# Kernel optimization log

Measured on AMD Instinct MI355X. Metric: run time of the kernel, lower is better.

The kernel has to match this reference:

```python
import jax, jax.numpy as jnp
import numpy as np

N, E, F, H, C1 = 50000, 1_600_000, 48, 1, 16  # nodes, edges, in_feats, heads, conv out


def setup_inputs() -> dict:
    key = jax.random.key(0)
    ks = jax.random.split(key, 12)
    in_ = jax.random.normal(ks[0], (N, F), dtype=jnp.float32)
    edge_index = jax.random.randint(ks[1], (2, E), 0, N, dtype=jnp.int64)
    labels = jax.random.bernoulli(ks[2], 0.5, (N, 1)).astype(jnp.float32)
    weights = jax.random.uniform(ks[3], (N, 1), dtype=jnp.float32) + 0.5
    s = 0.1  # PyG FeaStConv init: normal(0, 0.1)
    W = jax.random.normal(ks[4], (F, H * C1), dtype=jnp.float32) * s
    u = jax.random.normal(ks[5], (F, H), dtype=jnp.float32) * s
    c = jax.random.normal(ks[6], (H,), dtype=jnp.float32) * s
    bias = jax.random.normal(ks[7], (C1,), dtype=jnp.float32) * s
    lin1_w = jax.random.normal(ks[8], (C1, 8), dtype=jnp.float32) * (1.0 / np.sqrt(C1))
    lin1_b = jnp.zeros((8,), dtype=jnp.float32)
    out_w = jax.random.normal(ks[9], (8, 1), dtype=jnp.float32) * (1.0 / np.sqrt(8))
    out_b = jnp.zeros((1,), dtype=jnp.float32)
    return {"in_": in_, "edge_index": edge_index, "labels": labels,
            "weights": weights, "W": W, "u": u, "c": c, "bias": bias,
            "lin1_w": lin1_w, "lin1_b": lin1_b, "out_w": out_w, "out_b": out_b}


def feast_conv(x, edge_index, W, u, c, bias):
    n = x.shape[0]
    loop = jnp.arange(n, dtype=edge_index.dtype)  # add_self_loops=True
    src = jnp.concatenate([edge_index[0], loop])
    dst = jnp.concatenate([edge_index[1], loop])
    xj = x[src]                                   # [E+N, F] gather
    xi = x[dst]
    q = jax.nn.softmax((xj - xi) @ u + c, axis=-1)            # [E+N, H]
    xw = (xj @ W).reshape(-1, H, C1)                           # [E+N, H, C1]
    msg = jnp.einsum('ehc,eh->ec', xw, q)                      # [E+N, C1]
    agg = jax.ops.segment_sum(msg, dst, num_segments=n)        # scatter-sum
    deg = jax.ops.segment_sum(jnp.ones_like(dst, dtype=x.dtype), dst, num_segments=n)
    return agg / jnp.maximum(deg, 1.0)[:, None] + bias         # mean aggregation


def reference(in_, edge_index, labels, weights, W, u, c, bias, lin1_w, lin1_b, out_w, out_b):
    x = jax.nn.relu(feast_conv(in_, edge_index, W, u, c, bias))
    x = jax.nn.relu(x @ lin1_w + lin1_b)
    p = jax.nn.sigmoid(x @ out_w + out_b)                      # [N, 1]
    eps = 1e-7
    pc = jnp.clip(p, eps, 1.0 - eps)
    bce = -(labels * jnp.log(pc) + (1.0 - labels) * jnp.log(1.0 - pc))
    loss = jnp.mean(weights * bce)
    return (loss, p)
```

## Files before the change

kernel.cpp:

```cpp
#include <hip/hip_runtime.h>

constexpr int N_NODES  = 50000;
constexpr int N_EDGES  = 1600000;
constexpr int F_IN     = 48;
constexpr int C1_OUT   = 16;

constexpr int BNODES    = 128;
constexpr int NBINS     = 391;
constexpr int FILL_BLKS = 256;
constexpr int EPB       = N_EDGES / FILL_BLKS;
constexpr int SCAP      = 32;
constexpr int OCAP      = 8192;
constexpr int BIN_INTS  = FILL_BLKS * SCAP;
constexpr int LCAP      = 6144;

constexpr size_t OCNT_OFF   = 0;
constexpr size_t OFLOW_OFF  = 256;
constexpr size_t PART_OFF   = OFLOW_OFF + (size_t)OCAP * 4;
constexpr size_t XW_OFF     = PART_OFF + 4096;
constexpr size_t GSLOT_OFF  = XW_OFF + (size_t)N_NODES * C1_OUT * 4;
constexpr size_t GSLOT_BYTES = (size_t)NBINS * BIN_INTS * 4;

__device__ __forceinline__ void xw_body(int n, const float* __restrict__ x,
                                        const float* __restrict__ W,
                                        float* __restrict__ xw)
{
    const float4* xr = (const float4*)(x + (long)n * F_IN);
    float h[C1_OUT];
    #pragma unroll
    for (int c = 0; c < C1_OUT; ++c) h[c] = 0.f;
    #pragma unroll
    for (int k = 0; k < F_IN / 4; ++k) {
        float4 v = xr[k];
        #pragma unroll
        for (int c = 0; c < C1_OUT; ++c) {
            h[c] = fmaf(v.x, W[(4*k+0)*C1_OUT + c],
                   fmaf(v.y, W[(4*k+1)*C1_OUT + c],
                   fmaf(v.z, W[(4*k+2)*C1_OUT + c],
                   fmaf(v.w, W[(4*k+3)*C1_OUT + c], h[c]))));
        }
    }
    float4* o = (float4*)(xw + (long)n * C1_OUT);
    o[0] = make_float4(h[0],  h[1],  h[2],  h[3]);
    o[1] = make_float4(h[4],  h[5],  h[6],  h[7]);
    o[2] = make_float4(h[8],  h[9],  h[10], h[11]);
    o[3] = make_float4(h[12], h[13], h[14], h[15]);
}

constexpr int XW_BLKS = 49;

__global__ __launch_bounds__(1024)
void k_fill_xw(const int* __restrict__ src, const int* __restrict__ dst,
               int* __restrict__ gslot, int* __restrict__ ocnt,
               unsigned int* __restrict__ oflow,
               const float* __restrict__ x, const float* __restrict__ W,
               float* __restrict__ xw)
{
    __shared__ int lcnt[NBINS];

    if (blockIdx.x >= FILL_BLKS) {
        int n = (blockIdx.x - FILL_BLKS) * 1024 + threadIdx.x;
        if (n < N_NODES) xw_body(n, x, W, xw);
        return;
    }

    int tid = threadIdx.x;
    if (tid < NBINS) lcnt[tid] = 0;
    __syncthreads();

    int e0 = blockIdx.x * EPB;
    for (int i = tid; i < EPB; i += 1024) {
        int e = e0 + i;
        int s = src[e], d = dst[e];
        int b = d >> 7;
        int p = atomicAdd(&lcnt[b], 1);
        if (p < SCAP) {
            gslot[(size_t)(b * FILL_BLKS + blockIdx.x) * SCAP + p] = (s << 7) | (d & 127);
        } else {
            int g = atomicAdd(ocnt, 1);
            if (g < OCAP) oflow[g] = ((unsigned)s << 16) | (unsigned)d;
        }
    }
}

__device__ __forceinline__ float node_epilogue(
    float4 a, int n, float inv, const float* __restrict__ xw,
    const float* __restrict__ bias, const float* __restrict__ lin1_w,
    const float* __restrict__ lin1_b, const float* __restrict__ out_w,
    const float* __restrict__ out_b, const float* __restrict__ labels,
    const float* __restrict__ weights, float* __restrict__ out,
    float* s16, int lane)
{
    if (lane < 4) {
        float4 v  = ((const float4*)(xw + (size_t)n * C1_OUT))[lane];
        float4 b4 = ((const float4*)bias)[lane];
        float4 h;
        h.x = fmaxf(fmaf(a.x + v.x, inv, b4.x), 0.f);
        h.y = fmaxf(fmaf(a.y + v.y, inv, b4.y), 0.f);
        h.z = fmaxf(fmaf(a.z + v.z, inv, b4.z), 0.f);
        h.w = fmaxf(fmaf(a.w + v.w, inv, b4.w), 0.f);
        ((float4*)s16)[lane] = h;
    }
    float x2 = 0.f;
    if (lane < 8) {
        x2 = lin1_b[lane];
        #pragma unroll
        for (int k = 0; k < C1_OUT; ++k)
            x2 = fmaf(s16[k], lin1_w[k * 8 + lane], x2);
        x2 = fmaxf(x2, 0.f) * out_w[lane];
    }
    x2 += __shfl_xor(x2, 1, 64);
    x2 += __shfl_xor(x2, 2, 64);
    x2 += __shfl_xor(x2, 4, 64);
    float ret = 0.f;
    if (lane == 0) {
        float z = x2 + out_b[0];
        float p = 1.f / (1.f + __expf(-z));
        out[1 + n] = p;
        const float eps = 1e-7f;
        float pc = fminf(fmaxf(p, eps), 1.f - eps);
        float y  = labels[n];
        ret = weights[n] * (-(y * __logf(pc) + (1.f - y) * __logf(1.f - pc)));
    }
    return ret;
}

__global__ __launch_bounds__(512)
void k_agg(const int* __restrict__ gslot, const int* __restrict__ ocnt,
           const unsigned int* __restrict__ oflow, const float* __restrict__ xw,
           const float* __restrict__ bias, const float* __restrict__ lin1_w,
           const float* __restrict__ lin1_b, const float* __restrict__ out_w,
           const float* __restrict__ out_b, const float* __restrict__ labels,
           const float* __restrict__ weights, float* __restrict__ out,
           float* __restrict__ partials)
{
    __shared__ int   hist[BNODES];
    __shared__ int   cursor[BNODES];
    __shared__ unsigned short lbuk[LCAP];
    __shared__ float s16[8][16];
    __shared__ float sLossW[8];
    __shared__ int   sHalf;

    int B = blockIdx.x, tid = threadIdx.x, lane = tid & 63, w = tid >> 6;

    if (tid < BNODES) hist[tid] = 0;
    __syncthreads();

    const int4* sp = (const int4*)(gslot + (size_t)B * BIN_INTS);
    int4 q0 = sp[tid], q1 = sp[tid + 512], q2 = sp[tid + 1024], q3 = sp[tid + 1536];

    int oc = *ocnt; if (oc > OCAP) oc = OCAP;

    #define H1(v) if ((v) >= 0) atomicAdd(&hist[(v) & 127], 1)
    H1(q0.x); H1(q0.y); H1(q0.z); H1(q0.w);
    H1(q1.x); H1(q1.y); H1(q1.z); H1(q1.w);
    H1(q2.x); H1(q2.y); H1(q2.z); H1(q2.w);
    H1(q3.x); H1(q3.y); H1(q3.z); H1(q3.w);
    #undef H1
    for (int i = tid; i < oc; i += 512) {
        int d = (int)(oflow[i] & 0xffffu);
        if ((d >> 7) == B) atomicAdd(&hist[d & 127], 1);
    }
    __syncthreads();

    if (tid < 128) {
        int val = hist[tid];
        int s = val;
        #pragma unroll
        for (int off = 1; off < 64; off <<= 1) {
            int u = __shfl_up(s, off, 64);
            if (lane >= off) s += u;
        }
        cursor[tid] = s - val;
        if (tid == 63) sHalf = s;
    }
    __syncthreads();
    if (tid >= 64 && tid < 128) cursor[tid] += sHalf;
    __syncthreads();

    #define SC(v) if ((v) >= 0) { int p = atomicAdd(&cursor[(v) & 127], 1); \
                                  if (p < LCAP) lbuk[p] = (unsigned short)((unsigned)(v) >> 7); }
    SC(q0.x); SC(q0.y); SC(q0.z); SC(q0.w);
    SC(q1.x); SC(q1.y); SC(q1.z); SC(q1.w);
    SC(q2.x); SC(q2.y); SC(q2.z); SC(q2.w);
    SC(q3.x); SC(q3.y); SC(q3.z); SC(q3.w);
    #undef SC
    for (int i = tid; i < oc; i += 512) {
        unsigned v = oflow[i];
        int d = (int)(v & 0xffffu);
        if ((d >> 7) == B) {
            int p = atomicAdd(&cursor[d & 127], 1);
            if (p < LCAP) lbuk[p] = (unsigned short)(v >> 16);
        }
    }
    __syncthreads();

    int rslot = lane >> 2, c4 = lane & 3;
    float lossw = 0.f;
    for (int i = 0; i < 16; ++i) {
        int ln = w * 16 + i;
        int n = B * BNODES + ln;
        if (n >= N_NODES) break;
        int deg   = hist[ln];
        int start = cursor[ln] - deg;
        float4 a = make_float4(0.f, 0.f, 0.f, 0.f);
        for (int j0 = 0; j0 < deg; j0 += 16) {
            int j = j0 + rslot;
            if (j < deg && start + j < LCAP) {
                int s = lbuk[start + j];
                float4 v = ((const float4*)(xw + (size_t)s * C1_OUT))[c4];
                a.x += v.x; a.y += v.y; a.z += v.z; a.w += v.w;
            }
        }
        #pragma unroll
        for (int off = 4; off < 64; off <<= 1) {
            a.x += __shfl_xor(a.x, off, 64);
            a.y += __shfl_xor(a.y, off, 64);
            a.z += __shfl_xor(a.z, off, 64);
            a.w += __shfl_xor(a.w, off, 64);
        }
        lossw += node_epilogue(a, n, 1.f / (float)(deg + 1), xw, bias, lin1_w,
                               lin1_b, out_w, out_b, labels, weights, out,
                               s16[w], lane);
    }
    if (lane == 0) sLossW[w] = lossw;
    __syncthreads();
    if (tid == 0) {
        float t = 0.f;
        #pragma unroll
        for (int k = 0; k < 8; ++k) t += sLossW[k];
        partials[B] = t;
    }
}

__global__ __launch_bounds__(512)
void k_loss_final(const float* __restrict__ partials, float* __restrict__ out)
{
    __shared__ float sw[8];
    int tid = threadIdx.x, lane = tid & 63, wv = tid >> 6;
    float s = (tid < NBINS) ? partials[tid] : 0.f;
    #pragma unroll
    for (int off = 32; off > 0; off >>= 1) s += __shfl_down(s, off, 64);
    if (lane == 0) sw[wv] = s;
    __syncthreads();
    if (tid == 0) {
        float t = 0.f;
        #pragma unroll
        for (int k = 0; k < 8; ++k) t += sw[k];
        out[0] = t / (float)N_NODES;
    }
}

extern "C" void kernel_launch(void* const* d_in, const int* in_sizes, int n_in,
                              void* d_out, int out_size, void* d_ws, size_t ws_size,
                              hipStream_t stream)
{
    const float* x       = (const float*)d_in[0];
    const int*   eidx    = (const int*)  d_in[1];
    const float* labels  = (const float*)d_in[2];
    const float* weights = (const float*)d_in[3];
    const float* W       = (const float*)d_in[4];
    const float* bias    = (const float*)d_in[7];
    const float* lin1_w  = (const float*)d_in[8];
    const float* lin1_b  = (const float*)d_in[9];
    const float* out_w   = (const float*)d_in[10];
    const float* out_b   = (const float*)d_in[11];
    float* out = (float*)d_out;

    const int* src = eidx;
    const int* dst = eidx + N_EDGES;
    char* ws = (char*)d_ws;

    int*          ocnt     = (int*)(ws + OCNT_OFF);
    unsigned int* oflow    = (unsigned int*)(ws + OFLOW_OFF);
    float*        partials = (float*)(ws + PART_OFF);
    float*        xw       = (float*)(ws + XW_OFF);
    int*          gslot    = (int*)(ws + GSLOT_OFF);

    hipMemsetAsync(ocnt, 0, sizeof(int), stream);
    hipMemsetAsync(gslot, 0xFF, GSLOT_BYTES, stream);
    k_fill_xw<<<FILL_BLKS + XW_BLKS, 1024, 0, stream>>>(
        src, dst, gslot, ocnt, oflow, x, W, xw);
    k_agg<<<NBINS, 512, 0, stream>>>(
        gslot, ocnt, oflow, xw, bias, lin1_w, lin1_b,
        out_w, out_b, labels, weights, out, partials);
    k_loss_final<<<1, 512, 0, stream>>>(partials, out);
}
```

Baseline: 149.8 us.

## Replace gslot memset with per-slot counts and halve destination bin size

Removes the 0xFF memset of the whole slot buffer. The fill kernel now writes a byte count per (bin, fill-block) cell, and the aggregation kernel uses those counts to tell which slots are valid. Bins are halved to 64 nodes, with 782 aggregation blocks of 256 threads and slot capacity 16. This cuts memset bandwidth and shrinks shared-memory buckets, but more edges may spill into the global overflow list, which every block scans, and there are more blocks.

New measurement: 158.2 us. 1.06x slower.

```diff
diff --git a/kernel.cpp b/kernel.cpp
--- a/kernel.cpp
+++ b/kernel.cpp
@@ -5,21 +5,22 @@
 constexpr int F_IN     = 48;
 constexpr int C1_OUT   = 16;
 
-constexpr int BNODES    = 128;
-constexpr int NBINS     = 391;
+constexpr int BNODES    = 64;
+constexpr int NBINS     = 782;
 constexpr int FILL_BLKS = 256;
 constexpr int EPB       = N_EDGES / FILL_BLKS;
-constexpr int SCAP      = 32;
+constexpr int SCAP      = 16;
 constexpr int OCAP      = 8192;
 constexpr int BIN_INTS  = FILL_BLKS * SCAP;
-constexpr int LCAP      = 6144;
-
-constexpr size_t OCNT_OFF   = 0;
-constexpr size_t OFLOW_OFF  = 256;
-constexpr size_t PART_OFF   = OFLOW_OFF + (size_t)OCAP * 4;
-constexpr size_t XW_OFF     = PART_OFF + 4096;
-constexpr size_t GSLOT_OFF  = XW_OFF + (size_t)N_NODES * C1_OUT * 4;
-constexpr size_t GSLOT_BYTES = (size_t)NBINS * BIN_INTS * 4;
+constexpr int LCAP      = 2600;
+constexpr int XW_BLKS   = 49;
+
+constexpr size_t OCNT_OFF  = 0;
+constexpr size_t OFLOW_OFF = 256;
+constexpr size_t PART_OFF  = OFLOW_OFF + (size_t)OCAP * 4;
+constexpr size_t XW_OFF    = PART_OFF + 4096;
+constexpr size_t CNT_OFF   = XW_OFF + (size_t)N_NODES * C1_OUT * 4;
+constexpr size_t GSLOT_OFF = CNT_OFF + (size_t)NBINS * FILL_BLKS;
 
 __device__ __forceinline__ void xw_body(int n, const float* __restrict__ x,
                                         const float* __restrict__ W,
@@ -47,12 +48,10 @@
     o[3] = make_float4(h[12], h[13], h[14], h[15]);
 }
 
-constexpr int XW_BLKS = 49;
-
 __global__ __launch_bounds__(1024)
 void k_fill_xw(const int* __restrict__ src, const int* __restrict__ dst,
-               int* __restrict__ gslot, int* __restrict__ ocnt,
-               unsigned int* __restrict__ oflow,
+               int* __restrict__ gslot, unsigned char* __restrict__ cnt2d,
+               int* __restrict__ ocnt, unsigned int* __restrict__ oflow,
                const float* __restrict__ x, const float* __restrict__ W,
                float* __restrict__ xw)
 {
@@ -72,14 +71,20 @@
     for (int i = tid; i < EPB; i += 1024) {
         int e = e0 + i;
         int s = src[e], d = dst[e];
-        int b = d >> 7;
+        int b = d >> 6;
         int p = atomicAdd(&lcnt[b], 1);
         if (p < SCAP) {
-            gslot[(size_t)(b * FILL_BLKS + blockIdx.x) * SCAP + p] = (s << 7) | (d & 127);
+            gslot[((size_t)b * FILL_BLKS + blockIdx.x) * SCAP + p] = (s << 6) | (d & 63);
         } else {
             int g = atomicAdd(ocnt, 1);
             if (g < OCAP) oflow[g] = ((unsigned)s << 16) | (unsigned)d;
         }
+    }
+    __syncthreads();
+    for (int b = tid; b < NBINS; b += 1024) {
+        int c = lcnt[b];
+        cnt2d[(size_t)b * FILL_BLKS + blockIdx.x] =
+            (unsigned char)((c < SCAP) ? c : SCAP);
     }
 }
 
@@ -125,9 +130,10 @@
     return ret;
 }
 
-__global__ __launch_bounds__(512)
-void k_agg(const int* __restrict__ gslot, const int* __restrict__ ocnt,
-           const unsigned int* __restrict__ oflow, const float* __restrict__ xw,
+__global__ __launch_bounds__(256)
+void k_agg(const int* __restrict__ gslot, const unsigned char* __restrict__ cnt2d,
+           const int* __restrict__ ocnt, const unsigned int* __restrict__ oflow,
+           const float* __restrict__ xw,
            const float* __restrict__ bias, const float* __restrict__ lin1_w,
            const float* __restrict__ lin1_b, const float* __restrict__ out_w,
            const float* __restrict__ out_b, const float* __restrict__ labels,
@@ -136,34 +142,39 @@
 {
     __shared__ int   hist[BNODES];
     __shared__ int   cursor[BNODES];
+    __shared__ int   scnt[FILL_BLKS];
     __shared__ unsigned short lbuk[LCAP];
-    __shared__ float s16[8][16];
-    __shared__ float sLossW[8];
-    __shared__ int   sHalf;
+    __shared__ float s16[4][16];
+    __shared__ float sLossW[4];
 
     int B = blockIdx.x, tid = threadIdx.x, lane = tid & 63, w = tid >> 6;
 
     if (tid < BNODES) hist[tid] = 0;
+    scnt[tid] = cnt2d[(size_t)B * FILL_BLKS + tid];
     __syncthreads();
 
     const int4* sp = (const int4*)(gslot + (size_t)B * BIN_INTS);
-    int4 q0 = sp[tid], q1 = sp[tid + 512], q2 = sp[tid + 1024], q3 = sp[tid + 1536];
+    int4 q0 = sp[tid], q1 = sp[tid + 256], q2 = sp[tid + 512], q3 = sp[tid + 768];
+    int r0 = scnt[(tid)          >> 2] - ((tid & 3) << 2);
+    int r1 = scnt[(tid + 256)    >> 2] - ((tid & 3) << 2);
+    int r2 = scnt[(tid + 512)    >> 2] - ((tid & 3) << 2);
+    int r3 = scnt[(tid + 768)    >> 2] - ((tid & 3) << 2);
 
     int oc = *ocnt; if (oc > OCAP) oc = OCAP;
 
-    #define H1(v) if ((v) >= 0) atomicAdd(&hist[(v) & 127], 1)
-    H1(q0.x); H1(q0.y); H1(q0.z); H1(q0.w);
-    H1(q1.x); H1(q1.y); H1(q1.z); H1(q1.w);
-    H1(q2.x); H1(q2.y); H1(q2.z); H1(q2.w);
-    H1(q3.x); H1(q3.y); H1(q3.z); H1(q3.w);
-    #undef H1
-    for (int i = tid; i < oc; i += 512) {
+    #define H4(q, r) { if (0 < (r)) atomicAdd(&hist[(q).x & 63], 1); \
+                       if (1 < (r)) atomicAdd(&hist[(q).y & 63], 1); \
+                       if (2 < (r)) atomicAdd(&hist[(q).z & 63], 1); \
+                       if (3 < (r)) atomicAdd(&hist[(q).w & 63], 1); }
+    H4(q0, r0); H4(q1, r1); H4(q2, r2); H4(q3, r3);
+    #undef H4
+    for (int i = tid; i < oc; i += 256) {
         int d = (int)(oflow[i] & 0xffffu);
-        if ((d >> 7) == B) atomicAdd(&hist[d & 127], 1);
-    }
-    __syncthreads();
-
-    if (tid < 128) {
+        if ((d >> 6) == B) atomicAdd(&hist[d & 63], 1);
+    }
+    __syncthreads();
+
+    if (tid < 64) {
         int val = hist[tid];
         int s = val;
         #pragma unroll
@@ -172,27 +183,24 @@
             if (lane >= off) s += u;
         }
         cursor[tid] = s - val;
-        if (tid == 63) sHalf = s;
-    }
-    __syncthreads();
-    if (tid >= 64 && tid < 128) cursor[tid] += sHalf;
-    __syncthreads();
-
-    #define SC(v) if ((v) >= 0) { int p = atomicAdd(&cursor[(v) & 127], 1); \
-                                  if (p < LCAP) lbuk[p] = (unsigned short)((unsigned)(v) >> 7); }
-    SC(q0.x); SC(q0.y); SC(q0.z); SC(q0.w);
-    SC(q1.x); SC(q1.y); SC(q1.z); SC(q1.w);
-    SC(q2.x); SC(q2.y); SC(q2.z); SC(q2.w);
-    SC(q3.x); SC(q3.y); SC(q3.z); SC(q3.w);
-    #undef SC
-    for (int i = tid; i < oc; i += 512) {
+    }
+    __syncthreads();
+
+    #define SC1(v) { int p = atomicAdd(&cursor[(v) & 63], 1); \
+                     if (p < LCAP) lbuk[p] = (unsigned short)((unsigned)(v) >> 6); }
+    #define SC4(q, r) { if (0 < (r)) SC1((q).x); if (1 < (r)) SC1((q).y); \
+                        if (2 < (r)) SC1((q).z); if (3 < (r)) SC1((q).w); }
+    SC4(q0, r0); SC4(q1, r1); SC4(q2, r2); SC4(q3, r3);
+    #undef SC4
+    for (int i = tid; i < oc; i += 256) {
         unsigned v = oflow[i];
         int d = (int)(v & 0xffffu);
-        if ((d >> 7) == B) {
-            int p = atomicAdd(&cursor[d & 127], 1);
+        if ((d >> 6) == B) {
+            int p = atomicAdd(&cursor[d & 63], 1);
             if (p < LCAP) lbuk[p] = (unsigned short)(v >> 16);
         }
     }
+    #undef SC1
     __syncthreads();
 
     int rslot = lane >> 2, c4 = lane & 3;
@@ -225,18 +233,14 @@
     }
     if (lane == 0) sLossW[w] = lossw;
     __syncthreads();
-    if (tid == 0) {
-        float t = 0.f;
-        #pragma unroll
-        for (int k = 0; k < 8; ++k) t += sLossW[k];
-        partials[B] = t;
-    }
-}
-
-__global__ __launch_bounds__(512)
+    if (tid == 0)
+        partials[B] = sLossW[0] + sLossW[1] + sLossW[2] + sLossW[3];
+}
+
+__global__ __launch_bounds__(1024)
 void k_loss_final(const float* __restrict__ partials, float* __restrict__ out)
 {
-    __shared__ float sw[8];
+    __shared__ float sw[16];
     int tid = threadIdx.x, lane = tid & 63, wv = tid >> 6;
     float s = (tid < NBINS) ? partials[tid] : 0.f;
     #pragma unroll
@@ -246,7 +250,7 @@
     if (tid == 0) {
         float t = 0.f;
         #pragma unroll
-        for (int k = 0; k < 8; ++k) t += sw[k];
+        for (int k = 0; k < 16; ++k) t += sw[k];
         out[0] = t / (float)N_NODES;
     }
 }
@@ -271,18 +275,18 @@
     const int* dst = eidx + N_EDGES;
     char* ws = (char*)d_ws;
 
-    int*          ocnt     = (int*)(ws + OCNT_OFF);
-    unsigned int* oflow    = (unsigned int*)(ws + OFLOW_OFF);
-    float*        partials = (float*)(ws + PART_OFF);
-    float*        xw       = (float*)(ws + XW_OFF);
-    int*          gslot    = (int*)(ws + GSLOT_OFF);
+    int*           ocnt     = (int*)(ws + OCNT_OFF);
+    unsigned int*  oflow    = (unsigned int*)(ws + OFLOW_OFF);
+    float*         partials = (float*)(ws + PART_OFF);
+    float*         xw       = (float*)(ws + XW_OFF);
+    unsigned char* cnt2d    = (unsigned char*)(ws + CNT_OFF);
+    int*           gslot    = (int*)(ws + GSLOT_OFF);
 
     hipMemsetAsync(ocnt, 0, sizeof(int), stream);
-    hipMemsetAsync(gslot, 0xFF, GSLOT_BYTES, stream);
     k_fill_xw<<<FILL_BLKS + XW_BLKS, 1024, 0, stream>>>(
-        src, dst, gslot, ocnt, oflow, x, W, xw);
-    k_agg<<<NBINS, 512, 0, stream>>>(
-        gslot, ocnt, oflow, xw, bias, lin1_w, lin1_b,
+        src, dst, gslot, cnt2d, ocnt, oflow, x, W, xw);
+    k_agg<<<NBINS, 256, 0, stream>>>(
+        gslot, cnt2d, ocnt, oflow, xw, bias, lin1_w, lin1_b,
         out_w, out_b, labels, weights, out, partials);
-    k_loss_final<<<1, 512, 0, stream>>>(partials, out);
-}
+    k_loss_final<<<1, 1024, 0, stream>>>(partials, out);
+}
```
